# Kernel tuning notes

Hardware: AMD Instinct MI355X
Metric: run time of the kernel (lower is better)

## Reference

```python
import jax, jax.numpy as jnp
import numpy as np

B, L, HID = 2, 2048, 4096
NH, NKV, HD = 16, 4, 64
BLOCK = 16
THETA = 8000000.0
EPS = 1e-6
NEG = jnp.finfo(jnp.float32).min


def _rope_tables(theta, L, hd):
    inv_freq = 1.0 / (theta ** (np.arange(0, hd, 2, dtype=np.float32) / hd))  # [hd/2]
    t = np.arange(L, dtype=np.float32)
    freqs = np.outer(t, inv_freq)                      # [L, hd/2]
    emb = np.concatenate([freqs, freqs], axis=-1)      # [L, hd]
    return jnp.asarray(np.cos(emb)), jnp.asarray(np.sin(emb))


def setup_inputs() -> dict:
    key = jax.random.key(0)
    k1, k2, k3 = jax.random.split(key, 3)
    hidden_states = jax.random.normal(k1, (B, L, HID), dtype=jnp.float32)
    Wqkv = jax.random.normal(k2, (HID, (NH + 2 * NKV) * HD), dtype=jnp.float32) * 0.006
    Wo = jax.random.normal(k3, (NH * HD, HID), dtype=jnp.float32) * 0.006
    q_norm_w = jnp.ones((HD,), dtype=jnp.float32)
    k_norm_w = jnp.ones((HD,), dtype=jnp.float32)
    # block-diagonal causal additive mask [1,1,L,L]
    idx = jnp.arange(L)
    same_block = (idx[:, None] // BLOCK) == (idx[None, :] // BLOCK)
    causal = idx[:, None] >= idx[None, :]
    attention_mask = jnp.where(same_block & causal, 0.0, NEG)[None, None].astype(jnp.float32)
    cos1, sin1 = _rope_tables(THETA, L, HD)
    cos = jnp.broadcast_to(cos1[None], (B, L, HD))
    sin = jnp.broadcast_to(sin1[None], (B, L, HD))
    return {"hidden_states": hidden_states, "attention_mask": attention_mask,
            "cos": cos, "sin": sin, "Wqkv": Wqkv, "Wo": Wo,
            "q_norm_w": q_norm_w, "k_norm_w": k_norm_w}


def _rms_norm(x, w):
    xf = x.astype(jnp.float32)
    var = jnp.mean(xf * xf, axis=-1, keepdims=True)
    return (xf * jax.lax.rsqrt(var + EPS)).astype(x.dtype) * w


def _rotate_half(x):
    x1, x2 = jnp.split(x, 2, axis=-1)
    return jnp.concatenate([-x2, x1], axis=-1)


def reference(hidden_states, attention_mask, cos, sin, Wqkv, Wo, q_norm_w, k_norm_w):
    Bc, Lc, _ = hidden_states.shape
    qkv = hidden_states @ Wqkv                                # [B,L,(NH+2NKV)*HD]
    qkv = qkv.reshape(Bc, Lc, NH + 2 * NKV, HD)
    q, k, v = jnp.split(qkv, [NH, NH + NKV], axis=2)
    q = q.transpose(0, 2, 1, 3)                               # [B,NH,L,HD]
    k = k.transpose(0, 2, 1, 3)                               # [B,NKV,L,HD]
    v = v.transpose(0, 2, 1, 3)
    q = _rms_norm(q, q_norm_w)
    k = _rms_norm(k, k_norm_w)
    c = cos[:, None]                                          # [B,1,L,HD]
    s = sin[:, None]
    q = q * c + _rotate_half(q) * s
    k = k * c + _rotate_half(k) * s
    groups = NH // NKV
    k = jnp.repeat(k, groups, axis=1)                         # [B,NH,L,HD]
    v = jnp.repeat(v, groups, axis=1)
    scale = 1.0 / jnp.sqrt(jnp.float32(HD))
    scores = jnp.einsum('bhqd,bhkd->bhqk', q, k) * scale + attention_mask
    probs = jax.nn.softmax(scores, axis=-1)
    out = jnp.einsum('bhqk,bhkd->bhqd', probs, v)             # [B,NH,L,HD]
    out = out.transpose(0, 2, 1, 3).reshape(Bc, Lc, NH * HD)
    return out @ Wo
```

## Files before the change

### kernel.cpp

```cpp
#include <hip/hip_runtime.h>
#include <hip/hip_bf16.h>
#include <cstdint>

#define B_SZ   2
#define L_SEQ  2048
#define HID    4096
#define NH     16
#define NKV    4
#define HD     64
#define NQKV   (NH + 2*NKV)
#define QKV_N  (NQKV*HD)
#define O_N    (NH*HD)
#define M_ROWS (B_SZ*L_SEQ)
#define EPSV   1e-6f

typedef __bf16  bf16x8_t  __attribute__((ext_vector_type(8)));
typedef float   f32x4_t   __attribute__((ext_vector_type(4)));
typedef unsigned short ushort8_t __attribute__((ext_vector_type(8)));

__device__ __forceinline__ unsigned short f2b(float f) {
    union { float f; uint32_t u; } v; v.f = f;
    uint32_t r = v.u + 0x7FFFu + ((v.u >> 16) & 1u);
    return (unsigned short)(r >> 16);
}
__device__ __forceinline__ float b2f(unsigned short u) {
    union { uint32_t u; float f; } v; v.u = ((uint32_t)u) << 16;
    return v.f;
}

__device__ __forceinline__ void gload_lds16(const void* g, void* l) {
    __builtin_amdgcn_global_load_lds(
        (__attribute__((address_space(1))) void*)(g),
        (__attribute__((address_space(3))) void*)(l),
        16, 0, 0);
}

#define BARF() do { asm volatile("" ::: "memory"); \
                    __builtin_amdgcn_s_barrier();  \
                    asm volatile("" ::: "memory"); } while (0)
#define LGKM0() do { asm volatile("s_waitcnt lgkmcnt(0)" ::: "memory"); \
                     __builtin_amdgcn_sched_barrier(0); } while (0)
#define VMC6()  asm volatile("s_waitcnt vmcnt(6)" ::: "memory")
#define VMC4()  asm volatile("s_waitcnt vmcnt(4)" ::: "memory")
#define VMC0()  asm volatile("s_waitcnt vmcnt(0)" ::: "memory")

__global__ __launch_bounds__(256) void cvt_f32_bf16(const float* __restrict__ in,
                                                    unsigned short* __restrict__ out,
                                                    int n8) {
    int i = blockIdx.x * 256 + threadIdx.x;
    if (i >= n8) return;
    const float4* p = (const float4*)(in + (size_t)i * 8);
    float4 a = p[0], b = p[1];
    ushort8_t o;
    o[0]=f2b(a.x); o[1]=f2b(a.y); o[2]=f2b(a.z); o[3]=f2b(a.w);
    o[4]=f2b(b.x); o[5]=f2b(b.y); o[6]=f2b(b.z); o[7]=f2b(b.w);
    *(ushort8_t*)(out + (size_t)i * 8) = o;
}

__global__ __launch_bounds__(256) void transpose_f32_bf16(const float* __restrict__ in,
                                                          unsigned short* __restrict__ out,
                                                          int R, int C) {
    __shared__ float t[32][33];
    const int c0 = blockIdx.x * 32;
    const int r0 = blockIdx.y * 32;
    const int tx = threadIdx.x & 31;
    const int ty = threadIdx.x >> 5;
    #pragma unroll
    for (int i = 0; i < 32; i += 8)
        t[ty + i][tx] = in[(size_t)(r0 + ty + i) * C + c0 + tx];
    __syncthreads();
    #pragma unroll
    for (int i = 0; i < 32; i += 8)
        out[(size_t)(c0 + ty + i) * R + r0 + tx] = f2b(t[tx][ty + i]);
}

__global__ __launch_bounds__(512, 2) void gemm256_bf16(const unsigned short* __restrict__ A,
                                                       const unsigned short* __restrict__ Bt,
                                                       float* __restrict__ C,
                                                       int M, int N, int K) {
    __shared__ unsigned short smem[65536];

    const int tid  = threadIdx.x;
    const int lane = tid & 63;
    const int wave = tid >> 6;
    const int wr   = wave >> 2;
    const int wc   = wave & 3;
    const int fr   = lane & 15;
    const int fq   = lane >> 4;

    const int nbx = N >> 8;
    int bid = blockIdx.x;
    const int cpx = gridDim.x >> 3;
    bid = (bid & 7) * cpx + (bid >> 3);
    const int bx = bid % nbx, by = bid / nbx;
    const int m0 = by << 8, n0 = bx << 8;

    const int srow = tid >> 3;
    const int scs  = ((tid & 7) ^ (srow & 7)) << 3;
    const unsigned short* gA = A  + (size_t)(m0 + srow) * K + scs;
    const unsigned short* gB = Bt + (size_t)(n0 + srow) * K + scs;

    const int cx0 = ((fq)     ^ (fr & 7)) << 3;
    const int cx1 = ((4 | fq) ^ (fr & 7)) << 3;

    f32x4_t acc[8][4];
    #pragma unroll
    for (int m = 0; m < 8; m++)
        #pragma unroll
        for (int n = 0; n < 4; n++)
            acc[m][n] = (f32x4_t){0.f, 0.f, 0.f, 0.f};

    bf16x8_t aF[2][2];
    bf16x8_t bF[4][2];

#define STG_A2(T, H) { _Pragma("unroll") for (int q = 0; q < 2; ++q) \
    gload_lds16(gA + (size_t)((H)*128 + q*64) * K + ((size_t)(T) << 6), \
                &smem[(((T)&1)<<15) + ((H)*128 + q*64)*64 + tid*8]); }
#define STG_B2(T, H) { _Pragma("unroll") for (int q = 0; q < 2; ++q) \
    gload_lds16(gB + (size_t)((H)*128 + q*64) * K + ((size_t)(T) << 6), \
                &smem[(((T)&1)<<15) + 16384 + ((H)*128 + q*64)*64 + tid*8]); }
#define RD_B2(SB) { _Pragma("unroll") for (int nn = 0; nn < 4; ++nn) { \
    const int ro = (SB) + 16384 + (wc*64 + nn*16 + fr)*64; \
    bF[nn][0] = *(const bf16x8_t*)&smem[ro + cx0]; \
    bF[nn][1] = *(const bf16x8_t*)&smem[ro + cx1]; } }
#define RD_A2(SB, P) { _Pragma("unroll") for (int m2 = 0; m2 < 2; ++m2) { \
    const int ro = (SB) + (wr*128 + ((P)*2 + m2)*16 + fr)*64; \
    aF[m2][0] = *(const bf16x8_t*)&smem[ro + cx0]; \
    aF[m2][1] = *(const bf16x8_t*)&smem[ro + cx1]; } }
#define MM2(P) { __builtin_amdgcn_s_setprio(1); \
    _Pragma("unroll") for (int m2 = 0; m2 < 2; ++m2) \
    _Pragma("unroll") for (int nn = 0; nn < 4; ++nn) \
    _Pragma("unroll") for (int kk = 0; kk < 2; ++kk) \
        acc[(P)*2 + m2][nn] = __builtin_amdgcn_mfma_f32_16x16x32_bf16( \
            aF[m2][kk], bF[nn][kk], acc[(P)*2 + m2][nn], 0, 0, 0); \
    __builtin_amdgcn_s_setprio(0); }

    const int NT = K >> 6;
    STG_A2(0, 0); STG_A2(0, 1); STG_B2(0, 0); STG_B2(0, 1);
    STG_B2(1, 0); STG_B2(1, 1);
    VMC4();
    BARF();

    for (int t = 0; t < NT; ++t) {
        const int sb = (t & 1) << 15;
        RD_B2(sb); RD_A2(sb, 0);
        if (t + 1 < NT) STG_A2(t + 1, 0);
        BARF(); LGKM0(); MM2(0); BARF();
        RD_A2(sb, 1);
        if (t + 1 < NT) STG_A2(t + 1, 1);
        BARF(); LGKM0(); MM2(1); BARF();
        RD_A2(sb, 2);
        if (t + 2 < NT) STG_B2(t + 2, 0);
        BARF(); LGKM0(); MM2(2); BARF();
        RD_A2(sb, 3);
        if (t + 2 < NT) STG_B2(t + 2, 1);
        BARF(); LGKM0(); MM2(3);
        if (t + 2 < NT) { VMC4(); } else { VMC0(); }
        BARF();
    }

    const int crow = m0 + wr * 128 + fq * 4;
    const int ccol = n0 + wc * 64 + fr;
    #pragma unroll
    for (int m = 0; m < 8; m++)
        #pragma unroll
        for (int n = 0; n < 4; n++)
            #pragma unroll
            for (int rr = 0; rr < 4; rr++)
                C[(size_t)(crow + m*16 + rr) * N + ccol + n*16] = acc[m][n][rr];
#undef STG_A2
#undef STG_B2
#undef RD_B2
#undef RD_A2
#undef MM2
}

__global__ __launch_bounds__(512, 2) void gemm256x128_bf16(const unsigned short* __restrict__ A,
                                                           const unsigned short* __restrict__ Bt,
                                                           unsigned short* __restrict__ C,
                                                           int M, int N, int K) {
    __shared__ unsigned short smem[73728];

    const int tid  = threadIdx.x;
    const int lane = tid & 63;
    const int wave = tid >> 6;
    const int wq   = wave >> 1;
    const int wn   = wave & 1;
    const int fr   = lane & 15;
    const int fq   = lane >> 4;

    const int nbx = N >> 7;
    int bid = blockIdx.x;
    const int cpx = gridDim.x >> 3;
    bid = (bid & 7) * cpx + (bid >> 3);
    const int bx = bid % nbx, by = bid / nbx;
    const int m0 = by << 8, n0 = bx << 7;

    const int srow = tid >> 3;
    const int scs  = ((tid & 7) ^ (srow & 7)) << 3;
    const unsigned short* gA = A  + (size_t)(m0 + srow) * K + scs;
    const unsigned short* gB = Bt + (size_t)(n0 + srow) * K + scs;

    const int cx0 = ((fq)     ^ (fr & 7)) << 3;
    const int cx1 = ((4 | fq) ^ (fr & 7)) << 3;

    f32x4_t acc[4][4];
    #pragma unroll
    for (int m = 0; m < 4; m++)
        #pragma unroll
        for (int n = 0; n < 4; n++)
            acc[m][n] = (f32x4_t){0.f, 0.f, 0.f, 0.f};

    bf16x8_t aF[4][2];
    bf16x8_t bF[2][2];

#define STG_T1(T) { const int pb = ((T)%3)*24576; \
    _Pragma("unroll") for (int q = 0; q < 4; ++q) \
        gload_lds16(gA + (size_t)(q*64)*K + ((size_t)(T) << 6), \
                    &smem[pb + q*4096 + tid*8]); \
    _Pragma("unroll") for (int q = 0; q < 2; ++q) \
        gload_lds16(gB + (size_t)(q*64)*K + ((size_t)(T) << 6), \
                    &smem[pb + 16384 + q*4096 + tid*8]); }
#define RD_A1(SB) { _Pragma("unroll") for (int mm = 0; mm < 4; ++mm) { \
    const int ro = (SB) + (wq*64 + mm*16 + fr)*64; \
    aF[mm][0] = *(const bf16x8_t*)&smem[ro + cx0]; \
    aF[mm][1] = *(const bf16x8_t*)&smem[ro + cx1]; } }
#define RD_B1(SB, NN) { _Pragma("unroll") for (int n2 = 0; n2 < 2; ++n2) { \
    const int ro = (SB) + 16384 + (wn*64 + ((NN) + n2)*16 + fr)*64; \
    bF[n2][0] = *(const bf16x8_t*)&smem[ro + cx0]; \
    bF[n2][1] = *(const bf16x8_t*)&smem[ro + cx1]; } }
#define MM1(NH_) { __builtin_amdgcn_s_setprio(1); \
    _Pragma("unroll") for (int mm = 0; mm < 4; ++mm) \
    _Pragma("unroll") for (int n2 = 0; n2 < 2; ++n2) \
    _Pragma("unroll") for (int kk = 0; kk < 2; ++kk) \
        acc[mm][(NH_)*2 + n2] = __builtin_amdgcn_mfma_f32_16x16x32_bf16( \
            aF[mm][kk], bF[n2][kk], acc[mm][(NH_)*2 + n2], 0, 0, 0); \
    __builtin_amdgcn_s_setprio(0); }

    const int NT = K >> 6;
    STG_T1(0);
    STG_T1(1);
    VMC6();
    BARF();

    for (int t = 0; t < NT; ++t) {
        const int sb = (t % 3) * 24576;
        RD_A1(sb); RD_B1(sb, 0);
        if (t + 2 < NT) STG_T1(t + 2);
        BARF(); LGKM0(); MM1(0); BARF();
        RD_B1(sb, 2);
        BARF(); LGKM0(); MM1(1);
        if (t + 2 < NT) { VMC6(); } else if (t + 1 < NT) { VMC0(); }
        BARF();
    }

    const int crow = m0 + wq * 64 + fq * 4;
    const int ccol = n0 + wn * 64 + fr;
    #pragma unroll
    for (int m = 0; m < 4; m++)
        #pragma unroll
        for (int n = 0; n < 4; n++)
            #pragma unroll
            for (int rr = 0; rr < 4; rr++)
                C[(size_t)(crow + m*16 + rr) * N + ccol + n*16] = f2b(acc[m][n][rr]);
#undef STG_T1
#undef RD_A1
#undef RD_B1
#undef MM1
}

__global__ __launch_bounds__(64) void attn_fused(const unsigned short* __restrict__ qkv,
                                                 const float* __restrict__ cosb,
                                                 const float* __restrict__ sinb,
                                                 const float* __restrict__ qw,
                                                 const float* __restrict__ kw,
                                                 unsigned short* __restrict__ out) {
    const int h    = blockIdx.x & (NH - 1);
    const int blk  = (blockIdx.x >> 4) & 127;
    const int b    = blockIdx.x >> 11;
    const int pos0 = blk * 16;
    const int kvh  = h >> 2;

    const int lane = threadIdx.x;
    const int r    = lane >> 2;
    const int qp   = lane & 3;
    const int d0   = qp * 16;

    __shared__ float qs[16][65];
    __shared__ float ks[16][65];
    __shared__ float vs[16][65];
    __shared__ float ps[16][17];

    const size_t rowb = ((size_t)(b * L_SEQ + pos0 + r)) * NQKV;
    const unsigned short* qptr = qkv + (rowb + h) * HD + d0;
    const unsigned short* kptr = qkv + (rowb + NH + kvh) * HD + d0;
    const unsigned short* vptr = qkv + (rowb + NH + NKV + kvh) * HD + d0;
    const size_t csrow = ((size_t)(b * L_SEQ + pos0 + r)) * HD + d0;

    float q[16], k[16], v[16], cs[16], sn[16];
    {
        ushort8_t q0 = *(const ushort8_t*)&qptr[0], q1 = *(const ushort8_t*)&qptr[8];
        ushort8_t k0 = *(const ushort8_t*)&kptr[0], k1 = *(const ushort8_t*)&kptr[8];
        ushort8_t v0 = *(const ushort8_t*)&vptr[0], v1 = *(const ushort8_t*)&vptr[8];
        #pragma unroll
        for (int i = 0; i < 8; i++) {
            q[i] = b2f(q0[i]); q[i+8] = b2f(q1[i]);
            k[i] = b2f(k0[i]); k[i+8] = b2f(k1[i]);
            v[i] = b2f(v0[i]); v[i+8] = b2f(v1[i]);
        }
        #pragma unroll
        for (int i = 0; i < 16; i += 4) {
            *(float4*)&cs[i] = *(const float4*)&cosb[csrow + i];
            *(float4*)&sn[i] = *(const float4*)&sinb[csrow + i];
        }
    }

    float sq = 0.f, sk = 0.f;
    #pragma unroll
    for (int i = 0; i < 16; i++) { sq += q[i]*q[i]; sk += k[i]*k[i]; }
    sq += __shfl_xor(sq, 1); sq += __shfl_xor(sq, 2);
    sk += __shfl_xor(sk, 1); sk += __shfl_xor(sk, 2);
    const float rq = rsqrtf(sq * (1.f / HD) + EPSV);
    const float rk = rsqrtf(sk * (1.f / HD) + EPSV);

    const float sgn = (qp < 2) ? -1.f : 1.f;
    #pragma unroll
    for (int i = 0; i < 16; i++) {
        float qn = q[i] * rq * qw[d0 + i];
        float kn = k[i] * rk * kw[d0 + i];
        float qo = __shfl_xor(qn, 2);
        float ko = __shfl_xor(kn, 2);
        qs[r][d0 + i] = qn * cs[i] + sgn * qo * sn[i];
        ks[r][d0 + i] = kn * cs[i] + sgn * ko * sn[i];
        vs[r][d0 + i] = v[i];
    }
    __syncthreads();

    float sc[4] = {0.f, 0.f, 0.f, 0.f};
    for (int d = 0; d < 64; d++) {
        const float qd = qs[r][d];
        sc[0] += qd * ks[qp     ][d];
        sc[1] += qd * ks[qp +  4][d];
        sc[2] += qd * ks[qp +  8][d];
        sc[3] += qd * ks[qp + 12][d];
    }
    #pragma unroll
    for (int cc = 0; cc < 4; cc++) {
        const int c = qp + cc * 4;
        sc[cc] = (c <= r) ? sc[cc] * 0.125f : -3.0e38f;
    }
    float mx = fmaxf(fmaxf(sc[0], sc[1]), fmaxf(sc[2], sc[3]));
    mx = fmaxf(mx, __shfl_xor(mx, 1));
    mx = fmaxf(mx, __shfl_xor(mx, 2));
    float e[4], sum = 0.f;
    #pragma unroll
    for (int cc = 0; cc < 4; cc++) { e[cc] = __expf(sc[cc] - mx); sum += e[cc]; }
    sum += __shfl_xor(sum, 1); sum += __shfl_xor(sum, 2);
    const float inv = 1.f / sum;
    #pragma unroll
    for (int cc = 0; cc < 4; cc++) ps[r][qp + cc * 4] = e[cc] * inv;
    __syncthreads();

    float o[16];
    #pragma unroll
    for (int i = 0; i < 16; i++) o[i] = 0.f;
    #pragma unroll
    for (int c = 0; c < 16; c++) {
        const float p = ps[r][c];
        #pragma unroll
        for (int i = 0; i < 16; i++) o[i] += p * vs[c][d0 + i];
    }

    __attribute__((aligned(16))) unsigned short ob[16];
    #pragma unroll
    for (int i = 0; i < 16; i++) ob[i] = f2b(o[i]);
    unsigned short* optr = out + (((size_t)(b * L_SEQ + pos0 + r) * NH + h) * HD) + d0;
    *(uint4*)optr       = *(uint4*)&ob[0];
    *((uint4*)optr + 1) = *(uint4*)&ob[8];
}

extern "C" void kernel_launch(void* const* d_in, const int* in_sizes, int n_in,
                              void* d_out, int out_size, void* d_ws, size_t ws_size,
                              hipStream_t stream) {
    const float* hid  = (const float*)d_in[0];
    const float* cosb = (const float*)d_in[2];
    const float* sinb = (const float*)d_in[3];
    const float* Wqkv = (const float*)d_in[4];
    const float* Wo   = (const float*)d_in[5];
    const float* qw   = (const float*)d_in[6];
    const float* kw   = (const float*)d_in[7];
    float* outp = (float*)d_out;

    char* ws = (char*)d_ws;
    unsigned short* Hb    = (unsigned short*)ws; ws += (size_t)M_ROWS * HID * 2;
    unsigned short* WqkvT = (unsigned short*)ws; ws += (size_t)QKV_N * HID * 2;
    unsigned short* WoT   = (unsigned short*)ws; ws += (size_t)HID * O_N * 2;
    unsigned short* qkvb  = (unsigned short*)ws; ws += (size_t)M_ROWS * QKV_N * 2;
    unsigned short* attnb = (unsigned short*)ws;

    {
        int n8 = (M_ROWS * HID) / 8;
        cvt_f32_bf16<<<(n8 + 255) / 256, 256, 0, stream>>>(hid, Hb, n8);
    }
    transpose_f32_bf16<<<dim3(QKV_N / 32, HID / 32), 256, 0, stream>>>(Wqkv, WqkvT, HID, QKV_N);
    transpose_f32_bf16<<<dim3(HID / 32, O_N / 32),  256, 0, stream>>>(Wo,   WoT,   O_N, HID);
    gemm256x128_bf16<<<dim3((M_ROWS / 256) * (QKV_N / 128)), 512, 0, stream>>>(Hb, WqkvT, qkvb, M_ROWS, QKV_N, HID);
    attn_fused<<<dim3(B_SZ * (L_SEQ / 16) * NH), 64, 0, stream>>>(qkvb, cosb, sinb, qw, kw, attnb);
    gemm256_bf16<<<dim3((M_ROWS / 256) * (HID / 256)), 512, 0, stream>>>(attnb, WoT, outp, M_ROWS, HID, O_N);
}
```

Before: 160.6 us.

## Split GEMM main loops by K-half to cut fragment registers and rebalance stores

Both GEMM kernels now load LDS fragments one 32-wide K half at a time (cx0 then cx1) instead of both halves at once. This halves the A/B fragment register footprint and reorders the MFMA phases. The 256x128 kernel also splits its global-to-LDS staging into two parts spread over the two phases, and the 256x256 kernel issues both B stages together. The sched_barrier after the lgkmcnt wait is removed, which gives the compiler more freedom to schedule but may let it move instructions across the wait in unintended ways.

```diff
diff --git a/kernel.cpp b/kernel.cpp
--- a/kernel.cpp
+++ b/kernel.cpp
@@ -38,8 +38,7 @@
 #define BARF() do { asm volatile("" ::: "memory"); \
                     __builtin_amdgcn_s_barrier();  \
                     asm volatile("" ::: "memory"); } while (0)
-#define LGKM0() do { asm volatile("s_waitcnt lgkmcnt(0)" ::: "memory"); \
-                     __builtin_amdgcn_sched_barrier(0); } while (0)
+#define LGKMW() asm volatile("s_waitcnt lgkmcnt(0)" ::: "memory")
 #define VMC6()  asm volatile("s_waitcnt vmcnt(6)" ::: "memory")
 #define VMC4()  asm volatile("s_waitcnt vmcnt(4)" ::: "memory")
 #define VMC0()  asm volatile("s_waitcnt vmcnt(0)" ::: "memory")
@@ -110,8 +109,8 @@
         for (int n = 0; n < 4; n++)
             acc[m][n] = (f32x4_t){0.f, 0.f, 0.f, 0.f};
 
-    bf16x8_t aF[2][2];
-    bf16x8_t bF[4][2];
+    bf16x8_t aF[4];
+    bf16x8_t bFk[4];
 
 #define STG_A2(T, H) { _Pragma("unroll") for (int q = 0; q < 2; ++q) \
     gload_lds16(gA + (size_t)((H)*128 + q*64) * K + ((size_t)(T) << 6), \
@@ -119,20 +118,17 @@
 #define STG_B2(T, H) { _Pragma("unroll") for (int q = 0; q < 2; ++q) \
     gload_lds16(gB + (size_t)((H)*128 + q*64) * K + ((size_t)(T) << 6), \
                 &smem[(((T)&1)<<15) + 16384 + ((H)*128 + q*64)*64 + tid*8]); }
-#define RD_B2(SB) { _Pragma("unroll") for (int nn = 0; nn < 4; ++nn) { \
+#define RD_A2(SB, H, KX) { _Pragma("unroll") for (int mm = 0; mm < 4; ++mm) { \
+    const int ro = (SB) + (wr*128 + (H)*64 + mm*16 + fr)*64; \
+    aF[mm] = *(const bf16x8_t*)&smem[ro + (KX)]; } }
+#define RD_B2(SB, KX) { _Pragma("unroll") for (int nn = 0; nn < 4; ++nn) { \
     const int ro = (SB) + 16384 + (wc*64 + nn*16 + fr)*64; \
-    bF[nn][0] = *(const bf16x8_t*)&smem[ro + cx0]; \
-    bF[nn][1] = *(const bf16x8_t*)&smem[ro + cx1]; } }
-#define RD_A2(SB, P) { _Pragma("unroll") for (int m2 = 0; m2 < 2; ++m2) { \
-    const int ro = (SB) + (wr*128 + ((P)*2 + m2)*16 + fr)*64; \
-    aF[m2][0] = *(const bf16x8_t*)&smem[ro + cx0]; \
-    aF[m2][1] = *(const bf16x8_t*)&smem[ro + cx1]; } }
-#define MM2(P) { __builtin_amdgcn_s_setprio(1); \
-    _Pragma("unroll") for (int m2 = 0; m2 < 2; ++m2) \
+    bFk[nn] = *(const bf16x8_t*)&smem[ro + (KX)]; } }
+#define MM2(H) { __builtin_amdgcn_s_setprio(1); \
+    _Pragma("unroll") for (int mm = 0; mm < 4; ++mm) \
     _Pragma("unroll") for (int nn = 0; nn < 4; ++nn) \
-    _Pragma("unroll") for (int kk = 0; kk < 2; ++kk) \
-        acc[(P)*2 + m2][nn] = __builtin_amdgcn_mfma_f32_16x16x32_bf16( \
-            aF[m2][kk], bF[nn][kk], acc[(P)*2 + m2][nn], 0, 0, 0); \
+        acc[(H)*4 + mm][nn] = __builtin_amdgcn_mfma_f32_16x16x32_bf16( \
+            aF[mm], bFk[nn], acc[(H)*4 + mm][nn], 0, 0, 0); \
     __builtin_amdgcn_s_setprio(0); }
 
     const int NT = K >> 6;
@@ -143,18 +139,17 @@
 
     for (int t = 0; t < NT; ++t) {
         const int sb = (t & 1) << 15;
-        RD_B2(sb); RD_A2(sb, 0);
+        RD_A2(sb, 0, cx0); RD_B2(sb, cx0);
         if (t + 1 < NT) STG_A2(t + 1, 0);
-        BARF(); LGKM0(); MM2(0); BARF();
-        RD_A2(sb, 1);
+        BARF(); LGKMW(); MM2(0); BARF();
+        RD_A2(sb, 1, cx0);
         if (t + 1 < NT) STG_A2(t + 1, 1);
-        BARF(); LGKM0(); MM2(1); BARF();
-        RD_A2(sb, 2);
-        if (t + 2 < NT) STG_B2(t + 2, 0);
-        BARF(); LGKM0(); MM2(2); BARF();
-        RD_A2(sb, 3);
-        if (t + 2 < NT) STG_B2(t + 2, 1);
-        BARF(); LGKM0(); MM2(3);
+        BARF(); LGKMW(); MM2(1); BARF();
+        RD_A2(sb, 0, cx1); RD_B2(sb, cx1);
+        BARF(); LGKMW(); MM2(0); BARF();
+        RD_A2(sb, 1, cx1);
+        if (t + 2 < NT) { STG_B2(t + 2, 0); STG_B2(t + 2, 1); }
+        BARF(); LGKMW(); MM2(1);
         if (t + 2 < NT) { VMC4(); } else { VMC0(); }
         BARF();
     }
@@ -170,8 +165,8 @@
                 C[(size_t)(crow + m*16 + rr) * N + ccol + n*16] = acc[m][n][rr];
 #undef STG_A2
 #undef STG_B2
+#undef RD_A2
 #undef RD_B2
-#undef RD_A2
 #undef MM2
 }
 
@@ -211,45 +206,46 @@
         for (int n = 0; n < 4; n++)
             acc[m][n] = (f32x4_t){0.f, 0.f, 0.f, 0.f};
 
-    bf16x8_t aF[4][2];
-    bf16x8_t bF[2][2];
-
-#define STG_T1(T) { const int pb = ((T)%3)*24576; \
-    _Pragma("unroll") for (int q = 0; q < 4; ++q) \
+    bf16x8_t aF[4];
+    bf16x8_t bF[4];
+
+#define STG_T1a(T) { const int pb = ((T)%3)*24576; \
+    _Pragma("unroll") for (int q = 0; q < 3; ++q) \
         gload_lds16(gA + (size_t)(q*64)*K + ((size_t)(T) << 6), \
-                    &smem[pb + q*4096 + tid*8]); \
+                    &smem[pb + q*4096 + tid*8]); }
+#define STG_T1b(T) { const int pb = ((T)%3)*24576; \
+    gload_lds16(gA + (size_t)(3*64)*K + ((size_t)(T) << 6), \
+                &smem[pb + 3*4096 + tid*8]); \
     _Pragma("unroll") for (int q = 0; q < 2; ++q) \
         gload_lds16(gB + (size_t)(q*64)*K + ((size_t)(T) << 6), \
                     &smem[pb + 16384 + q*4096 + tid*8]); }
-#define RD_A1(SB) { _Pragma("unroll") for (int mm = 0; mm < 4; ++mm) { \
+#define RD_A1(SB, KX) { _Pragma("unroll") for (int mm = 0; mm < 4; ++mm) { \
     const int ro = (SB) + (wq*64 + mm*16 + fr)*64; \
-    aF[mm][0] = *(const bf16x8_t*)&smem[ro + cx0]; \
-    aF[mm][1] = *(const bf16x8_t*)&smem[ro + cx1]; } }
-#define RD_B1(SB, NN) { _Pragma("unroll") for (int n2 = 0; n2 < 2; ++n2) { \
-    const int ro = (SB) + 16384 + (wn*64 + ((NN) + n2)*16 + fr)*64; \
-    bF[n2][0] = *(const bf16x8_t*)&smem[ro + cx0]; \
-    bF[n2][1] = *(const bf16x8_t*)&smem[ro + cx1]; } }
-#define MM1(NH_) { __builtin_amdgcn_s_setprio(1); \
+    aF[mm] = *(const bf16x8_t*)&smem[ro + (KX)]; } }
+#define RD_B1(SB, KX) { _Pragma("unroll") for (int nn = 0; nn < 4; ++nn) { \
+    const int ro = (SB) + 16384 + (wn*64 + nn*16 + fr)*64; \
+    bF[nn] = *(const bf16x8_t*)&smem[ro + (KX)]; } }
+#define MM1() { __builtin_amdgcn_s_setprio(1); \
     _Pragma("unroll") for (int mm = 0; mm < 4; ++mm) \
-    _Pragma("unroll") for (int n2 = 0; n2 < 2; ++n2) \
-    _Pragma("unroll") for (int kk = 0; kk < 2; ++kk) \
-        acc[mm][(NH_)*2 + n2] = __builtin_amdgcn_mfma_f32_16x16x32_bf16( \
-            aF[mm][kk], bF[n2][kk], acc[mm][(NH_)*2 + n2], 0, 0, 0); \
+    _Pragma("unroll") for (int nn = 0; nn < 4; ++nn) \
+        acc[mm][nn] = __builtin_amdgcn_mfma_f32_16x16x32_bf16( \
+            aF[mm], bF[nn], acc[mm][nn], 0, 0, 0); \
     __builtin_amdgcn_s_setprio(0); }
 
     const int NT = K >> 6;
-    STG_T1(0);
-    STG_T1(1);
+    STG_T1a(0); STG_T1b(0);
+    STG_T1a(1); STG_T1b(1);
     VMC6();
     BARF();
 
     for (int t = 0; t < NT; ++t) {
         const int sb = (t % 3) * 24576;
-        RD_A1(sb); RD_B1(sb, 0);
-        if (t + 2 < NT) STG_T1(t + 2);
-        BARF(); LGKM0(); MM1(0); BARF();
-        RD_B1(sb, 2);
-        BARF(); LGKM0(); MM1(1);
+        RD_A1(sb, cx0); RD_B1(sb, cx0);
+        if (t + 2 < NT) STG_T1a(t + 2);
+        BARF(); LGKMW(); MM1(); BARF();
+        RD_A1(sb, cx1); RD_B1(sb, cx1);
+        if (t + 2 < NT) STG_T1b(t + 2);
+        BARF(); LGKMW(); MM1();
         if (t + 2 < NT) { VMC6(); } else if (t + 1 < NT) { VMC0(); }
         BARF();
     }
@@ -263,7 +259,8 @@
             #pragma unroll
             for (int rr = 0; rr < 4; rr++)
                 C[(size_t)(crow + m*16 + rr) * N + ccol + n*16] = f2b(acc[m][n][rr]);
-#undef STG_T1
+#undef STG_T1a
+#undef STG_T1b
 #undef RD_A1
 #undef RD_B1
 #undef MM1
```

Result: no change. 158.8 us (-1.1%).
